# Kernel tuning notes

Measured on AMD Instinct MI355X. Metric: run time of the kernel, lower is better.

## Reference

```python
import jax, jax.numpy as jnp
import numpy as np

D_MODEL = 1024
N_HEAD = 16
D_K = D_MODEL // N_HEAD
B, S = 4, 2048


def setup_inputs() -> dict:
    key = jax.random.key(0)
    ks = jax.random.split(key, 12)
    def w(k):
        return jax.random.normal(k, (D_MODEL, D_MODEL), dtype=jnp.float32) * 0.02
    def b(k):
        return jax.random.normal(k, (D_MODEL,), dtype=jnp.float32) * 0.02
    return {
        "x": jax.random.normal(ks[0], (B, S, D_MODEL), dtype=jnp.float32),
        "pos_emb": jax.random.normal(ks[1], (S, D_MODEL), dtype=jnp.float32),
        "Wq": w(ks[2]), "bq": b(ks[3]),
        "Wk": w(ks[4]), "bk": b(ks[5]),
        "Wv": w(ks[6]), "bv": b(ks[7]),
        "Wp": w(ks[8]), "bp": b(ks[9]),
        "Wo": w(ks[10]), "bo": b(ks[11]),
    }


def reference(x, pos_emb, Wq, bq, Wk, bk, Wv, bv, Wp, bp, Wo, bo):
    # x: [B, S, D]; pos_emb: [S, D]. cache=None path (prefill): kv_len == S.
    Bsz, Sl, _ = x.shape
    def heads(t):  # [B, S, D] -> [B, H, S, dk]
        return t.reshape(Bsz, Sl, N_HEAD, D_K).transpose(0, 2, 1, 3)
    q = heads(x @ Wq.T + bq)
    k = heads(x @ Wk.T + bk)
    v = heads(x @ Wv.T + bv)
    # pos projection: [S, D] -> [H, S, dk]
    p = (pos_emb @ Wp.T + bp).reshape(Sl, N_HEAD, D_K).transpose(1, 0, 2)
    q_pos = q + p[None]  # broadcast over batch
    scores = jnp.einsum("bhqd,bhkd->bhqk", q_pos, k) / jnp.sqrt(jnp.asarray(D_K, x.dtype))
    # causal mask: triu(ones(S, S), diagonal=1) positions are masked
    causal = jnp.tril(jnp.ones((Sl, Sl), dtype=bool))  # True = keep
    scores = jnp.where(causal[None, None], scores, -jnp.inf)
    attn = jax.nn.softmax(scores, axis=-1)  # dropout is identity (eval / p=0)
    out = jnp.einsum("bhqk,bhkd->bhqd", attn, v)
    out = out.transpose(0, 2, 1, 3).reshape(Bsz, Sl, D_MODEL)
    return out @ Wo.T + bo
```

## Files before the change

kernel.cpp:

```cpp
#include <hip/hip_runtime.h>

#define D_MODEL 1024
#define N_HEADS 16
#define DK 64
#define BATCH 4
#define SEQ 2048
#define MROWS (BATCH * SEQ)

typedef float f32x4 __attribute__((ext_vector_type(4)));
typedef short bf16x8 __attribute__((ext_vector_type(8)));
typedef unsigned short u16;
typedef unsigned short u16x8 __attribute__((ext_vector_type(8)));

__device__ __forceinline__ float bf2f(u16 u) {
    union { unsigned int i; float f; } v; v.i = ((unsigned int)u) << 16; return v.f;
}
__device__ __forceinline__ u16 f2bf(float f) {
    union { float f; unsigned int i; } v; v.f = f;
    unsigned int u = v.i;
    u += 0x7fffu + ((u >> 16) & 1u);
    return (u16)(u >> 16);
}
__device__ __forceinline__ unsigned int pk2(float a, float b) {
    union { float f; unsigned int i; } ua, ub; ua.f = a; ub.f = b;
    return __builtin_amdgcn_perm(ub.i + 0x8000u, ua.i + 0x8000u, 0x07060302u);
}

typedef unsigned int u32_as1 __attribute__((address_space(1)));
typedef unsigned int u32_as3 __attribute__((address_space(3)));
__device__ __forceinline__ void gload16(const u16* g, u16* l) {
    __builtin_amdgcn_global_load_lds((const u32_as1*)g, (u32_as3*)l, 16, 0, 0);
}

__global__ __launch_bounds__(256) void convert_all(
    const float* __restrict__ x, const float* __restrict__ pe,
    const float* __restrict__ w0, const float* __restrict__ w1, const float* __restrict__ w2,
    const float* __restrict__ w3, const float* __restrict__ w4,
    u16* __restrict__ xb, u16* __restrict__ pb,
    u16* __restrict__ wb0, u16* __restrict__ wb1, u16* __restrict__ wb2,
    u16* __restrict__ wb3, u16* __restrict__ wb4)
{
    int t = blockIdx.x * 256 + threadIdx.x;
    const float* src; u16* dst; int idx;
    if (t < 1048576)      { src = x;  dst = xb; idx = t; }
    else if (t < 1310720) { src = pe; dst = pb; idx = t - 1048576; }
    else {
        int r = t - 1310720; int w = r >> 17; idx = r & 131071;
        if      (w == 0) { src = w0; dst = wb0; }
        else if (w == 1) { src = w1; dst = wb1; }
        else if (w == 2) { src = w2; dst = wb2; }
        else if (w == 3) { src = w3; dst = wb3; }
        else             { src = w4; dst = wb4; }
    }
    const float4* p = (const float4*)src + (size_t)idx * 2;
    float4 a = p[0], b = p[1];
    u16x8 o;
    o[0] = f2bf(a.x); o[1] = f2bf(a.y); o[2] = f2bf(a.z); o[3] = f2bf(a.w);
    o[4] = f2bf(b.x); o[5] = f2bf(b.y); o[6] = f2bf(b.z); o[7] = f2bf(b.w);
    *((u16x8*)dst + idx) = o;
}

__global__ __launch_bounds__(256) void qkv_gemm(
    const u16* __restrict__ xb, const u16* __restrict__ peb,
    const u16* __restrict__ wqb, const u16* __restrict__ wkb,
    const u16* __restrict__ wvb, const u16* __restrict__ wpb,
    const float* __restrict__ bq, const float* __restrict__ bk,
    const float* __restrict__ bv, const float* __restrict__ bp,
    u16* __restrict__ Qb, u16* __restrict__ Kb, u16* __restrict__ V3,
    u16* __restrict__ Pb)
{
    __shared__ __align__(16) u16 As[128 * 32];
    __shared__ __align__(16) u16 Bs[128 * 32];

    const int tid  = threadIdx.x;
    const int lane = tid & 63;
    const int wv   = tid >> 6;
    const int l15  = lane & 15;
    const int quad = lane >> 4;
    int chunk, m0, n0;
    if (blockIdx.y < 24) {
        chunk = blockIdx.y >> 3; n0 = (blockIdx.y & 7) * 128; m0 = blockIdx.x * 128;
    } else {
        chunk = 3;
        int idx = (blockIdx.y - 24) * 64 + blockIdx.x;
        m0 = (idx & 15) * 128; n0 = ((idx >> 4) & 7) * 128;
    }
    const int wrow = (wv >> 1) * 64;
    const int wcol = (wv & 1) * 64;

    f32x4 acc[4][4];
#pragma unroll
    for (int i = 0; i < 4; ++i)
#pragma unroll
        for (int j = 0; j < 4; ++j) acc[i][j] = f32x4{0.f, 0.f, 0.f, 0.f};

    const int lr = lane >> 2;
    const int lc = (lane & 3) * 8;
    const u16* Abase = (chunk == 3) ? peb : xb;
    const u16* Wbase = (chunk == 0) ? wqb : ((chunk == 1) ? wkb : ((chunk == 2) ? wvb : wpb));
    const u16* Ag = Abase + (size_t)(m0 + wv * 16 + lr) * 1024 + lc;
    const u16* Wg = Wbase + (size_t)(n0 + wv * 16 + lr) * 1024 + lc;
    u16* Al = &As[wv * 16 * 32];
    u16* Bl = &Bs[wv * 16 * 32];

    for (int k0 = 0; k0 < 1024; k0 += 32) {
        __syncthreads();
        gload16(Ag + k0, Al);
        gload16(Ag + (size_t)64 * 1024 + k0, Al + 64 * 32);
        gload16(Wg + k0, Bl);
        gload16(Wg + (size_t)64 * 1024 + k0, Bl + 64 * 32);
        __syncthreads();

        bf16x8 af[4], bfr[4];
#pragma unroll
        for (int i = 0; i < 4; ++i)
            af[i] = *(const bf16x8*)&As[(wrow + 16 * i + l15) * 32 + quad * 8];
#pragma unroll
        for (int j = 0; j < 4; ++j)
            bfr[j] = *(const bf16x8*)&Bs[(wcol + 16 * j + l15) * 32 + quad * 8];
#pragma unroll
        for (int i = 0; i < 4; ++i)
#pragma unroll
            for (int j = 0; j < 4; ++j)
                acc[i][j] = __builtin_amdgcn_mfma_f32_16x16x32_bf16(af[i], bfr[j], acc[i][j], 0, 0, 0);
    }

    const int r0 = quad * 4;
    const float* bias = (chunk == 0) ? bq : ((chunk == 1) ? bk : ((chunk == 2) ? bv : bp));
    u16* dst = (chunk == 0) ? Qb : ((chunk == 1) ? Kb : Pb);
#pragma unroll
    for (int i = 0; i < 4; ++i) {
#pragma unroll
        for (int j = 0; j < 4; ++j) {
            int col = n0 + wcol + 16 * j + l15;
            int row0 = m0 + wrow + 16 * i + r0;
            float bvv = bias[col];
            if (chunk == 2) {
                int hh = col >> 6, d = col & 63;
                int bb = row0 >> 11, sl = row0 & 2047;
                union { u16 h[4]; uint2 v; } pk;
#pragma unroll
                for (int r = 0; r < 4; ++r) pk.h[r] = f2bf(acc[i][j][r] + bvv);
                *((uint2*)V3 + ((size_t)(bb * 16 + hh) * 512 + (sl >> 2)) * 64 + d) = pk.v;
            } else {
#pragma unroll
                for (int r = 0; r < 4; ++r)
                    dst[(size_t)(row0 + r) * 1024 + col] = f2bf(acc[i][j][r] + bvv);
            }
        }
    }
}

__global__ __launch_bounds__(256) void gemm_out(
    const u16* __restrict__ A, const u16* __restrict__ W,
    const float* __restrict__ bias, float* __restrict__ Cout)
{
    __shared__ __align__(16) u16 As[128 * 32];
    __shared__ __align__(16) u16 Bs[128 * 32];

    const int tid  = threadIdx.x;
    const int lane = tid & 63;
    const int wv   = tid >> 6;
    const int l15  = lane & 15;
    const int quad = lane >> 4;
    const int m0   = blockIdx.x * 128;
    const int n0   = blockIdx.y * 128;
    const int wrow = (wv >> 1) * 64;
    const int wcol = (wv & 1) * 64;

    f32x4 acc[4][4];
#pragma unroll
    for (int i = 0; i < 4; ++i)
#pragma unroll
        for (int j = 0; j < 4; ++j) acc[i][j] = f32x4{0.f, 0.f, 0.f, 0.f};

    const int lr = lane >> 2;
    const int lc = (lane & 3) * 8;
    const u16* Ag = A + (size_t)(m0 + wv * 16 + lr) * 1024 + lc;
    const u16* Wg = W + (size_t)(n0 + wv * 16 + lr) * 1024 + lc;
    u16* Al = &As[wv * 16 * 32];
    u16* Bl = &Bs[wv * 16 * 32];

    for (int k0 = 0; k0 < 1024; k0 += 32) {
        __syncthreads();
        gload16(Ag + k0, Al);
        gload16(Ag + 64 * 1024 + k0, Al + 64 * 32);
        gload16(Wg + k0, Bl);
        gload16(Wg + 64 * 1024 + k0, Bl + 64 * 32);
        __syncthreads();

        bf16x8 af[4], bfr[4];
#pragma unroll
        for (int i = 0; i < 4; ++i)
            af[i] = *(const bf16x8*)&As[(wrow + 16 * i + l15) * 32 + quad * 8];
#pragma unroll
        for (int j = 0; j < 4; ++j)
            bfr[j] = *(const bf16x8*)&Bs[(wcol + 16 * j + l15) * 32 + quad * 8];
#pragma unroll
        for (int i = 0; i < 4; ++i)
#pragma unroll
            for (int j = 0; j < 4; ++j)
                acc[i][j] = __builtin_amdgcn_mfma_f32_16x16x32_bf16(af[i], bfr[j], acc[i][j], 0, 0, 0);
    }

    const int r0 = quad * 4;
#pragma unroll
    for (int i = 0; i < 4; ++i)
#pragma unroll
        for (int j = 0; j < 4; ++j) {
            int col = n0 + wcol + 16 * j + l15;
            float bvv = bias[col];
#pragma unroll
            for (int r = 0; r < 4; ++r) {
                int row = m0 + wrow + 16 * i + r0 + r;
                Cout[(size_t)row * 1024 + col] = acc[i][j][r] + bvv;
            }
        }
}

__global__ __launch_bounds__(512, 4) void flash_attn_mfma(
    const u16* __restrict__ Q, const u16* __restrict__ Kq,
    const u16* __restrict__ V3, const u16* __restrict__ Pb, u16* __restrict__ O)
{
    __shared__ __align__(16) u16 Ks[64 * 72];
    __shared__ __align__(16) u16 Vs[64 * 72];
    __shared__ __align__(16) u16 Ps[8][32 * 72];

    const int tid  = threadIdx.x;
    const int lane = tid & 63;
    const int wv   = tid >> 6;
    const int l15  = lane & 15;
    const int quad = lane >> 4;
    const int j    = blockIdx.y;
    const int h    = blockIdx.x & 15;
    const int b    = blockIdx.x >> 4;
    const int qblk = (wv < 4) ? j : (15 - j);
    const int wq0  = qblk * 128 + (wv & 3) * 32;

    bf16x8 qf[2][2];
    const size_t qrowbase = (size_t)(b * SEQ) * D_MODEL + h * DK;
#pragma unroll
    for (int qb = 0; qb < 2; ++qb)
#pragma unroll
        for (int ks = 0; ks < 2; ++ks) {
            int qrow = wq0 + qb * 16 + l15;
            u16x8 qr = *(const u16x8*)(Q + qrowbase + (size_t)qrow * D_MODEL + ks * 32 + quad * 8);
            u16x8 pr = *(const u16x8*)(Pb + (size_t)qrow * D_MODEL + h * DK + ks * 32 + quad * 8);
            u16x8 o;
#pragma unroll
            for (int t = 0; t < 8; ++t)
                o[t] = f2bf((bf2f(qr[t]) + bf2f(pr[t])) * 0.180336880111120f);
            qf[qb][ks] = *(bf16x8*)&o;
        }

    f32x4 Oacc[2][4];
#pragma unroll
    for (int i = 0; i < 2; ++i)
#pragma unroll
        for (int jj = 0; jj < 4; ++jj) Oacc[i][jj] = f32x4{0.f, 0.f, 0.f, 0.f};
    float l_r[2] = {0.f, 0.f};

    const int sr  = tid >> 3;
    const int sc8 = (tid & 7) * 8;
    const u16* Kg = Kq + (size_t)(b * SEQ + sr) * D_MODEL + h * DK + sc8;
    const uint2* Vg = (const uint2*)V3 + ((size_t)(b * 16 + h) * 512 + (tid & 7) * 2) * 64 + sr;
    u16x8 kreg = *(const u16x8*)Kg;
    uint2 v0 = Vg[0], v1 = Vg[64];

    const int ktmaxb = 31 - 2 * j;
    for (int kt = 0; kt <= ktmaxb; ++kt) {
        __syncthreads();
        *(u16x8*)&Ks[sr * 72 + sc8] = kreg;
        *(uint2*)&Vs[sr * 72 + sc8] = v0;
        *(uint2*)&Vs[sr * 72 + sc8 + 4] = v1;
        __syncthreads();
        if (kt < ktmaxb) {
            kreg = *(const u16x8*)(Kg + (size_t)(kt + 1) * 64 * D_MODEL);
            v0 = Vg[(size_t)(kt + 1) * 1024];
            v1 = Vg[(size_t)(kt + 1) * 1024 + 64];
        }
        if (kt * 64 > wq0 + 31) continue;

        f32x4 sacc[4][2];
#pragma unroll
        for (int kb = 0; kb < 4; ++kb)
#pragma unroll
            for (int qb = 0; qb < 2; ++qb) sacc[kb][qb] = f32x4{0.f, 0.f, 0.f, 0.f};
#pragma unroll
        for (int ks = 0; ks < 2; ++ks) {
            bf16x8 kf[4];
#pragma unroll
            for (int kb = 0; kb < 4; ++kb)
                kf[kb] = *(const bf16x8*)&Ks[(kb * 16 + l15) * 72 + ks * 32 + quad * 8];
#pragma unroll
            for (int kb = 0; kb < 4; ++kb)
#pragma unroll
                for (int qb = 0; qb < 2; ++qb)
                    sacc[kb][qb] = __builtin_amdgcn_mfma_f32_16x16x32_bf16(kf[kb], qf[qb][ks], sacc[kb][qb], 0, 0, 0);
        }

        if (kt * 64 + 63 > wq0) {
#pragma unroll
            for (int kb = 0; kb < 4; ++kb) {
                int key_g = kt * 64 + kb * 16 + quad * 4;
#pragma unroll
                for (int qb = 0; qb < 2; ++qb) {
                    int q_g = wq0 + qb * 16 + l15;
#pragma unroll
                    for (int r = 0; r < 4; ++r)
                        if (key_g + r > q_g) sacc[kb][qb][r] = -1e30f;
                }
            }
        }

        u16* Pw = Ps[wv];
#pragma unroll
        for (int qb = 0; qb < 2; ++qb) {
            float s = 0.f;
#pragma unroll
            for (int kb = 0; kb < 4; ++kb) {
                float p0 = __builtin_amdgcn_exp2f(sacc[kb][qb][0]);
                float p1 = __builtin_amdgcn_exp2f(sacc[kb][qb][1]);
                float p2 = __builtin_amdgcn_exp2f(sacc[kb][qb][2]);
                float p3 = __builtin_amdgcn_exp2f(sacc[kb][qb][3]);
                s += (p0 + p1) + (p2 + p3);
                uint2 pk; pk.x = pk2(p0, p1); pk.y = pk2(p2, p3);
                *(uint2*)&Pw[(qb * 16 + l15) * 72 + kb * 16 + quad * 4] = pk;
            }
            l_r[qb] += s;
        }

#pragma unroll
        for (int ks = 0; ks < 2; ++ks) {
            bf16x8 pf[2], vf[4];
#pragma unroll
            for (int qb = 0; qb < 2; ++qb)
                pf[qb] = *(const bf16x8*)&Pw[(qb * 16 + l15) * 72 + ks * 32 + quad * 8];
#pragma unroll
            for (int db = 0; db < 4; ++db)
                vf[db] = *(const bf16x8*)&Vs[(db * 16 + l15) * 72 + ks * 32 + quad * 8];
#pragma unroll
            for (int qb = 0; qb < 2; ++qb)
#pragma unroll
                for (int db = 0; db < 4; ++db)
                    Oacc[qb][db] = __builtin_amdgcn_mfma_f32_16x16x32_bf16(pf[qb], vf[db], Oacc[qb][db], 0, 0, 0);
        }
    }

    float linv[2];
#pragma unroll
    for (int qb = 0; qb < 2; ++qb) {
        float s = l_r[qb];
        s += __shfl_xor(s, 16);
        s += __shfl_xor(s, 32);
        linv[qb] = 1.f / s;
    }
#pragma unroll
    for (int qb = 0; qb < 2; ++qb)
#pragma unroll
        for (int r = 0; r < 4; ++r) {
            float li = __shfl(linv[qb], quad * 4 + r);
            size_t row = (size_t)(b * SEQ + wq0 + qb * 16 + quad * 4 + r) * D_MODEL + h * DK;
#pragma unroll
            for (int db = 0; db < 4; ++db)
                O[row + db * 16 + l15] = f2bf(Oacc[qb][db][r] * li);
        }
}

extern "C" void kernel_launch(void* const* d_in, const int* in_sizes, int n_in,
                              void* d_out, int out_size, void* d_ws, size_t ws_size,
                              hipStream_t stream) {
    const float* x  = (const float*)d_in[0];
    const float* pe = (const float*)d_in[1];
    const float* Wq = (const float*)d_in[2];  const float* bq = (const float*)d_in[3];
    const float* Wk = (const float*)d_in[4];  const float* bk = (const float*)d_in[5];
    const float* Wv = (const float*)d_in[6];  const float* bv = (const float*)d_in[7];
    const float* Wp = (const float*)d_in[8];  const float* bp = (const float*)d_in[9];
    const float* Wo = (const float*)d_in[10]; const float* bo = (const float*)d_in[11];
    float* out = (float*)d_out;
    char* ws = (char*)d_ws;

    size_t off = 0;
    u16* xb  = (u16*)(ws + off); off += (size_t)MROWS * D_MODEL * 2;
    u16* peb = (u16*)(ws + off); off += (size_t)SEQ * D_MODEL * 2;
    u16* wqb = (u16*)(ws + off); off += (size_t)D_MODEL * D_MODEL * 2;
    u16* wkb = (u16*)(ws + off); off += (size_t)D_MODEL * D_MODEL * 2;
    u16* wvb = (u16*)(ws + off); off += (size_t)D_MODEL * D_MODEL * 2;
    u16* wpb = (u16*)(ws + off); off += (size_t)D_MODEL * D_MODEL * 2;
    u16* wob = (u16*)(ws + off); off += (size_t)D_MODEL * D_MODEL * 2;
    u16* Qb  = (u16*)(ws + off); off += (size_t)MROWS * D_MODEL * 2;
    u16* Kb  = (u16*)(ws + off); off += (size_t)MROWS * D_MODEL * 2;
    u16* V3b = (u16*)(ws + off); off += (size_t)MROWS * D_MODEL * 2;
    u16* Pb  = (u16*)(ws + off); off += (size_t)SEQ * D_MODEL * 2;
    u16* AO = xb;

    convert_all<<<7680, 256, 0, stream>>>(x, pe, Wq, Wk, Wv, Wp, Wo,
                                          xb, peb, wqb, wkb, wvb, wpb, wob);

    qkv_gemm<<<dim3(64, 26), 256, 0, stream>>>(
        xb, peb, wqb, wkb, wvb, wpb, bq, bk, bv, bp, Qb, Kb, V3b, Pb);

    flash_attn_mfma<<<dim3(64, 8), 512, 0, stream>>>(Qb, Kb, V3b, Pb, AO);

    gemm_out<<<dim3(64, 8), 256, 0, stream>>>(AO, wob, bo, out);
}
```

Baseline: 306.1 us.

## Double-buffer LDS tiles in QKV and output GEMMs to overlap loads with MFMA

Both the QKV projection GEMM and the output projection GEMM now use two LDS buffers per operand. The next K-slice is issued with async global-to-LDS loads while MFMAs run on the current slice, and there is one barrier per slice instead of two. This aims to hide global load latency behind compute. It doubles LDS usage per block, which may lower occupancy, and correctness depends on gload16 being asynchronous with proper waits at the barriers.

Result: slower. 313.7 us (+2.5%).

```diff
diff --git a/kernel.cpp b/kernel.cpp
--- a/kernel.cpp
+++ b/kernel.cpp
@@ -69,8 +69,8 @@
     u16* __restrict__ Qb, u16* __restrict__ Kb, u16* __restrict__ V3,
     u16* __restrict__ Pb)
 {
-    __shared__ __align__(16) u16 As[128 * 32];
-    __shared__ __align__(16) u16 Bs[128 * 32];
+    __shared__ __align__(16) u16 As[2][128 * 32];
+    __shared__ __align__(16) u16 Bs[2][128 * 32];
 
     const int tid  = threadIdx.x;
     const int lane = tid & 63;
@@ -100,29 +100,37 @@
     const u16* Wbase = (chunk == 0) ? wqb : ((chunk == 1) ? wkb : ((chunk == 2) ? wvb : wpb));
     const u16* Ag = Abase + (size_t)(m0 + wv * 16 + lr) * 1024 + lc;
     const u16* Wg = Wbase + (size_t)(n0 + wv * 16 + lr) * 1024 + lc;
-    u16* Al = &As[wv * 16 * 32];
-    u16* Bl = &Bs[wv * 16 * 32];
-
-    for (int k0 = 0; k0 < 1024; k0 += 32) {
-        __syncthreads();
-        gload16(Ag + k0, Al);
-        gload16(Ag + (size_t)64 * 1024 + k0, Al + 64 * 32);
-        gload16(Wg + k0, Bl);
-        gload16(Wg + (size_t)64 * 1024 + k0, Bl + 64 * 32);
-        __syncthreads();
-
+    const int woff = wv * 16 * 32;
+
+    auto stage = [&](int k, int buf) {
+        gload16(Ag + k, &As[buf][woff]);
+        gload16(Ag + (size_t)64 * 1024 + k, &As[buf][woff + 64 * 32]);
+        gload16(Wg + k, &Bs[buf][woff]);
+        gload16(Wg + (size_t)64 * 1024 + k, &Bs[buf][woff + 64 * 32]);
+    };
+    auto compute = [&](int buf) {
         bf16x8 af[4], bfr[4];
 #pragma unroll
         for (int i = 0; i < 4; ++i)
-            af[i] = *(const bf16x8*)&As[(wrow + 16 * i + l15) * 32 + quad * 8];
+            af[i] = *(const bf16x8*)&As[buf][(wrow + 16 * i + l15) * 32 + quad * 8];
 #pragma unroll
         for (int j = 0; j < 4; ++j)
-            bfr[j] = *(const bf16x8*)&Bs[(wcol + 16 * j + l15) * 32 + quad * 8];
+            bfr[j] = *(const bf16x8*)&Bs[buf][(wcol + 16 * j + l15) * 32 + quad * 8];
 #pragma unroll
         for (int i = 0; i < 4; ++i)
 #pragma unroll
             for (int j = 0; j < 4; ++j)
                 acc[i][j] = __builtin_amdgcn_mfma_f32_16x16x32_bf16(af[i], bfr[j], acc[i][j], 0, 0, 0);
+    };
+
+    stage(0, 0);
+    for (int k0 = 0; k0 < 1024; k0 += 64) {
+        __syncthreads();
+        stage(k0 + 32, 1);
+        compute(0);
+        __syncthreads();
+        if (k0 + 64 < 1024) stage(k0 + 64, 0);
+        compute(1);
     }
 
     const int r0 = quad * 4;
@@ -155,8 +163,8 @@
     const u16* __restrict__ A, const u16* __restrict__ W,
     const float* __restrict__ bias, float* __restrict__ Cout)
 {
-    __shared__ __align__(16) u16 As[128 * 32];
-    __shared__ __align__(16) u16 Bs[128 * 32];
+    __shared__ __align__(16) u16 As[2][128 * 32];
+    __shared__ __align__(16) u16 Bs[2][128 * 32];
 
     const int tid  = threadIdx.x;
     const int lane = tid & 63;
@@ -178,29 +186,37 @@
     const int lc = (lane & 3) * 8;
     const u16* Ag = A + (size_t)(m0 + wv * 16 + lr) * 1024 + lc;
     const u16* Wg = W + (size_t)(n0 + wv * 16 + lr) * 1024 + lc;
-    u16* Al = &As[wv * 16 * 32];
-    u16* Bl = &Bs[wv * 16 * 32];
-
-    for (int k0 = 0; k0 < 1024; k0 += 32) {
-        __syncthreads();
-        gload16(Ag + k0, Al);
-        gload16(Ag + 64 * 1024 + k0, Al + 64 * 32);
-        gload16(Wg + k0, Bl);
-        gload16(Wg + 64 * 1024 + k0, Bl + 64 * 32);
-        __syncthreads();
-
+    const int woff = wv * 16 * 32;
+
+    auto stage = [&](int k, int buf) {
+        gload16(Ag + k, &As[buf][woff]);
+        gload16(Ag + (size_t)64 * 1024 + k, &As[buf][woff + 64 * 32]);
+        gload16(Wg + k, &Bs[buf][woff]);
+        gload16(Wg + (size_t)64 * 1024 + k, &Bs[buf][woff + 64 * 32]);
+    };
+    auto compute = [&](int buf) {
         bf16x8 af[4], bfr[4];
 #pragma unroll
         for (int i = 0; i < 4; ++i)
-            af[i] = *(const bf16x8*)&As[(wrow + 16 * i + l15) * 32 + quad * 8];
+            af[i] = *(const bf16x8*)&As[buf][(wrow + 16 * i + l15) * 32 + quad * 8];
 #pragma unroll
         for (int j = 0; j < 4; ++j)
-            bfr[j] = *(const bf16x8*)&Bs[(wcol + 16 * j + l15) * 32 + quad * 8];
+            bfr[j] = *(const bf16x8*)&Bs[buf][(wcol + 16 * j + l15) * 32 + quad * 8];
 #pragma unroll
         for (int i = 0; i < 4; ++i)
 #pragma unroll
             for (int j = 0; j < 4; ++j)
                 acc[i][j] = __builtin_amdgcn_mfma_f32_16x16x32_bf16(af[i], bfr[j], acc[i][j], 0, 0, 0);
+    };
+
+    stage(0, 0);
+    for (int k0 = 0; k0 < 1024; k0 += 64) {
+        __syncthreads();
+        stage(k0 + 32, 1);
+        compute(0);
+        __syncthreads();
+        if (k0 + 64 < 1024) stage(k0 + 64, 0);
+        compute(1);
     }
 
     const int r0 = quad * 4;
```
